# Kernel tuning notes

Hardware: AMD Instinct MI355X
Metric: run time of the kernel (lower is better)

## Reference

```python
import jax, jax.numpy as jnp
import numpy as np

N_NODES = 100000
DEG = 16
N_EDGES = N_NODES * DEG
D_IN = 128
D_OUT = 128


def setup_inputs() -> dict:
    key = jax.random.key(0)
    k1, k2, k3 = jax.random.split(key, 3)
    X = jax.random.normal(k1, (N_NODES, D_IN), dtype=jnp.float32)
    weights = jax.random.normal(k2, (D_IN, D_OUT), dtype=jnp.float32) * (1.0 / np.sqrt(D_OUT))
    # fixed-degree CSR: row i owns edges [i*DEG, (i+1)*DEG)
    row_pointers = (jnp.arange(N_NODES + 1, dtype=jnp.int32) * DEG)
    column_index = jax.random.randint(k3, (N_EDGES,), 0, N_NODES, dtype=jnp.int32)
    # TC-GNN kernel-scheduling metadata (no effect on math)
    blockPartition = jnp.zeros((N_NODES // DEG,), dtype=jnp.int32)
    edgeToColumn = jnp.zeros((N_EDGES,), dtype=jnp.int32)
    edgeToRow = jnp.zeros((N_EDGES,), dtype=jnp.int32)
    return {"X": X, "weights": weights, "row_pointers": row_pointers,
            "column_index": column_index, "blockPartition": blockPartition,
            "edgeToColumn": edgeToColumn, "edgeToRow": edgeToRow}


def _csr_spmm(feat, row_pointers, column_index):
    # out[i] = sum_{e in row i} feat[column_index[e]]  (unweighted SpMM)
    n = row_pointers.shape[0] - 1
    e = column_index.shape[0]
    # map each edge to its source row via searchsorted on the CSR pointer array
    row_ids = jnp.searchsorted(row_pointers, jnp.arange(e, dtype=row_pointers.dtype), side='right') - 1
    gathered = feat[column_index]  # [E, D]
    return jax.ops.segment_sum(gathered, row_ids, num_segments=n)


def reference(X, weights, row_pointers, column_index, blockPartition, edgeToColumn, edgeToRow):
    X_prime = jnp.matmul(X, weights)                      # [N, D_OUT] dense GEMM
    return _csr_spmm(X_prime, row_pointers, column_index)  # [N, D_OUT] neighbor sum
```

## Files before the change

### kernel.cpp

```cpp
#include <hip/hip_runtime.h>
#include <hip/hip_bf16.h>

#define N_NODES 100000
#define DEG 16
#define D 128

typedef __bf16 bf16x8 __attribute__((ext_vector_type(8)));
typedef float f32x4 __attribute__((ext_vector_type(4)));

__device__ __forceinline__ unsigned pk2(float a, float b) {
  union { __bf16 h[2]; unsigned u; } x;
  x.h[0] = (__bf16)a; x.h[1] = (__bf16)b;
  return x.u;
}

__device__ __forceinline__ int swz(int row, int k) {
  return (row << 7) + (k ^ ((row & 7) << 3));
}

__global__ void k_convW(const float* __restrict__ W, ushort* __restrict__ Wt) {
  int pos = (blockIdx.x << 8) + threadIdx.x;
  int k = pos >> 7, n = pos & 127;
  union { __bf16 h; ushort u; } c;
  c.h = (__bf16)W[pos];
  Wt[swz(n, k)] = c.u;
}

__global__ __launch_bounds__(256, 2) void k_gemm(const float* __restrict__ X,
                                                 const ushort* __restrict__ Wt,
                                                 ushort* __restrict__ Xp) {
  __shared__ __align__(16) ushort Ws[128 * 128];
  const int tid = threadIdx.x;
  const int row0 = blockIdx.x << 7;
  const int wave = tid >> 6;
  const int lane = tid & 63;
  const int lhi = lane >> 4;
  const int llo = lane & 15;

  {
    const uint4* src = (const uint4*)Wt;
    uint4* dst = (uint4*)Ws;
#pragma unroll
    for (int j = 0; j < 8; ++j) dst[(j << 8) + tid] = src[(j << 8) + tid];
  }

  float4 xa[2][4][2];
#pragma unroll
  for (int m = 0; m < 2; ++m) {
    int row = row0 + (wave << 5) + (m << 4) + llo;
    const float* rp = X + row * D + (lhi << 3);
    bool ok = row < N_NODES;
#pragma unroll
    for (int t = 0; t < 4; ++t) {
      xa[m][t][0] = ok ? *(const float4*)(rp + (t << 5)) : make_float4(0.f, 0.f, 0.f, 0.f);
      xa[m][t][1] = ok ? *(const float4*)(rp + (t << 5) + 4) : make_float4(0.f, 0.f, 0.f, 0.f);
    }
  }
  __syncthreads();

  f32x4 acc[2][8];
#pragma unroll
  for (int m = 0; m < 2; ++m)
#pragma unroll
    for (int n = 0; n < 8; ++n)
      acc[m][n] = (f32x4){0.f, 0.f, 0.f, 0.f};

#pragma unroll
  for (int t = 0; t < 4; ++t) {
    const int k0 = (t << 5) + (lhi << 3);
    bf16x8 a[2], b[8];
#pragma unroll
    for (int m = 0; m < 2; ++m) {
      float4 p = xa[m][t][0], q = xa[m][t][1];
      bf16x8 v;
      v[0] = (__bf16)p.x; v[1] = (__bf16)p.y; v[2] = (__bf16)p.z; v[3] = (__bf16)p.w;
      v[4] = (__bf16)q.x; v[5] = (__bf16)q.y; v[6] = (__bf16)q.z; v[7] = (__bf16)q.w;
      a[m] = v;
    }
#pragma unroll
    for (int n = 0; n < 8; ++n)
      b[n] = *(const bf16x8*)(Ws + swz((n << 4) + llo, k0));
#pragma unroll
    for (int m = 0; m < 2; ++m)
#pragma unroll
      for (int n = 0; n < 8; ++n)
        acc[m][n] = __builtin_amdgcn_mfma_f32_16x16x32_bf16(a[m], b[n], acc[m][n], 0, 0, 0);
  }

#pragma unroll
  for (int m = 0; m < 2; ++m) {
#pragma unroll
    for (int r = 0; r < 4; ++r) {
      int row = row0 + (wave << 5) + (m << 4) + (lhi << 2) + r;
      if (row < N_NODES) {
        uint4 v;
        v.x = pk2(acc[m][0][r], acc[m][1][r]);
        v.y = pk2(acc[m][2][r], acc[m][3][r]);
        v.z = pk2(acc[m][4][r], acc[m][5][r]);
        v.w = pk2(acc[m][6][r], acc[m][7][r]);
        *(uint4*)(Xp + row * D + (llo << 3)) = v;
      }
    }
  }
}

__global__ __launch_bounds__(256) void k_spmm(const ushort* __restrict__ Xp,
                                              const int* __restrict__ ci,
                                              float* __restrict__ out) {
  const int wave = threadIdx.x >> 6;
  const int lane = threadIdx.x & 63;
  const int row = (blockIdx.x << 2) + wave;
  if (row >= N_NODES) return;
  const int g = lane >> 4;
  const int j = lane & 15;

  int idx = 0;
  if (lane < DEG) idx = __builtin_nontemporal_load(ci + row * DEG + lane);

  uint4 v[4];
#pragma unroll
  for (int e = 0; e < 4; ++e) {
    int col = __shfl(idx, (g << 2) + e);
    v[e] = *(const uint4*)(Xp + col * D + (j << 3));
  }

  float acc[8];
#pragma unroll
  for (int n = 0; n < 8; ++n) acc[n] = 0.f;
#pragma unroll
  for (int e = 0; e < 4; ++e) {
    acc[0] += __uint_as_float(v[e].x << 16);
    acc[1] += __uint_as_float(v[e].x & 0xffff0000u);
    acc[2] += __uint_as_float(v[e].y << 16);
    acc[3] += __uint_as_float(v[e].y & 0xffff0000u);
    acc[4] += __uint_as_float(v[e].z << 16);
    acc[5] += __uint_as_float(v[e].z & 0xffff0000u);
    acc[6] += __uint_as_float(v[e].w << 16);
    acc[7] += __uint_as_float(v[e].w & 0xffff0000u);
  }

#pragma unroll
  for (int n = 0; n < 8; ++n) {
    acc[n] += __shfl_xor(acc[n], 16);
    acc[n] += __shfl_xor(acc[n], 32);
  }

  float* op = out + row * D + (g << 5) + j;
  __builtin_nontemporal_store(acc[(g << 1)], op);
  __builtin_nontemporal_store(acc[(g << 1) + 1], op + 16);
}

extern "C" void kernel_launch(void* const* d_in, const int* in_sizes, int n_in,
                              void* d_out, int out_size, void* d_ws, size_t ws_size,
                              hipStream_t stream) {
  const float* X = (const float*)d_in[0];
  const float* W = (const float*)d_in[1];
  const int* ci = (const int*)d_in[3];

  ushort* Wt = (ushort*)d_ws;
  ushort* Xp = (ushort*)d_ws + 128 * 128;
  float* out = (float*)d_out;

  k_convW<<<64, 256, 0, stream>>>(W, Wt);
  k_gemm<<<(N_NODES + 127) / 128, 256, 0, stream>>>(X, Wt, Xp);
  k_spmm<<<N_NODES / 4, 256, 0, stream>>>(Xp, ci, out);
}
```

Measured before the change: 83.45 us.

## Halve GEMM rows per block and make SpMM persistent with index prefetch

The GEMM now handles 64 rows per block instead of 128, with one M-tile per wave, higher launch-bounds occupancy and nontemporal X loads. Each block still loads the whole 32KB W tile into shared memory, so twice as many blocks repeat that copy. The SpMM becomes a grid-stride persistent kernel with 2048 blocks that prefetches the next row's column indices while gathering the current row. The aims are better latency hiding in the GEMM and less block launch overhead in the SpMM, at the cost of extra redundant W staging and fewer waves in flight for the gather.

```diff
diff --git a/kernel.cpp b/kernel.cpp
--- a/kernel.cpp
+++ b/kernel.cpp
@@ -4,9 +4,11 @@
 #define N_NODES 100000
 #define DEG 16
 #define D 128
+#define SPMM_BLOCKS 2048
 
 typedef __bf16 bf16x8 __attribute__((ext_vector_type(8)));
 typedef float f32x4 __attribute__((ext_vector_type(4)));
+typedef float f32x4v __attribute__((ext_vector_type(4)));
 
 __device__ __forceinline__ unsigned pk2(float a, float b) {
   union { __bf16 h[2]; unsigned u; } x;
@@ -26,12 +28,12 @@
   Wt[swz(n, k)] = c.u;
 }
 
-__global__ __launch_bounds__(256, 2) void k_gemm(const float* __restrict__ X,
+__global__ __launch_bounds__(256, 4) void k_gemm(const float* __restrict__ X,
                                                  const ushort* __restrict__ Wt,
                                                  ushort* __restrict__ Xp) {
   __shared__ __align__(16) ushort Ws[128 * 128];
   const int tid = threadIdx.x;
-  const int row0 = blockIdx.x << 7;
+  const int row0 = blockIdx.x << 6;
   const int wave = tid >> 6;
   const int lane = tid & 63;
   const int lhi = lane >> 4;
@@ -44,62 +46,51 @@
     for (int j = 0; j < 8; ++j) dst[(j << 8) + tid] = src[(j << 8) + tid];
   }
 
-  float4 xa[2][4][2];
-#pragma unroll
-  for (int m = 0; m < 2; ++m) {
-    int row = row0 + (wave << 5) + (m << 4) + llo;
+  bf16x8 af[4];
+  {
+    int row = row0 + (wave << 4) + llo;
     const float* rp = X + row * D + (lhi << 3);
     bool ok = row < N_NODES;
+    f32x4v t0[4], t1[4];
 #pragma unroll
     for (int t = 0; t < 4; ++t) {
-      xa[m][t][0] = ok ? *(const float4*)(rp + (t << 5)) : make_float4(0.f, 0.f, 0.f, 0.f);
-      xa[m][t][1] = ok ? *(const float4*)(rp + (t << 5) + 4) : make_float4(0.f, 0.f, 0.f, 0.f);
+      t0[t] = ok ? __builtin_nontemporal_load((const f32x4v*)(rp + (t << 5))) : (f32x4v){0.f, 0.f, 0.f, 0.f};
+      t1[t] = ok ? __builtin_nontemporal_load((const f32x4v*)(rp + (t << 5) + 4)) : (f32x4v){0.f, 0.f, 0.f, 0.f};
+    }
+#pragma unroll
+    for (int t = 0; t < 4; ++t) {
+      bf16x8 v;
+      v[0] = (__bf16)t0[t][0]; v[1] = (__bf16)t0[t][1]; v[2] = (__bf16)t0[t][2]; v[3] = (__bf16)t0[t][3];
+      v[4] = (__bf16)t1[t][0]; v[5] = (__bf16)t1[t][1]; v[6] = (__bf16)t1[t][2]; v[7] = (__bf16)t1[t][3];
+      af[t] = v;
     }
   }
   __syncthreads();
 
-  f32x4 acc[2][8];
+  f32x4 acc[8];
 #pragma unroll
-  for (int m = 0; m < 2; ++m)
-#pragma unroll
-    for (int n = 0; n < 8; ++n)
-      acc[m][n] = (f32x4){0.f, 0.f, 0.f, 0.f};
+  for (int n = 0; n < 8; ++n) acc[n] = (f32x4){0.f, 0.f, 0.f, 0.f};
 
 #pragma unroll
   for (int t = 0; t < 4; ++t) {
     const int k0 = (t << 5) + (lhi << 3);
-    bf16x8 a[2], b[8];
 #pragma unroll
-    for (int m = 0; m < 2; ++m) {
-      float4 p = xa[m][t][0], q = xa[m][t][1];
-      bf16x8 v;
-      v[0] = (__bf16)p.x; v[1] = (__bf16)p.y; v[2] = (__bf16)p.z; v[3] = (__bf16)p.w;
-      v[4] = (__bf16)q.x; v[5] = (__bf16)q.y; v[6] = (__bf16)q.z; v[7] = (__bf16)q.w;
-      a[m] = v;
+    for (int n = 0; n < 8; ++n) {
+      bf16x8 b = *(const bf16x8*)(Ws + swz((n << 4) + llo, k0));
+      acc[n] = __builtin_amdgcn_mfma_f32_16x16x32_bf16(af[t], b, acc[n], 0, 0, 0);
     }
-#pragma unroll
-    for (int n = 0; n < 8; ++n)
-      b[n] = *(const bf16x8*)(Ws + swz((n << 4) + llo, k0));
-#pragma unroll
-    for (int m = 0; m < 2; ++m)
-#pragma unroll
-      for (int n = 0; n < 8; ++n)
-        acc[m][n] = __builtin_amdgcn_mfma_f32_16x16x32_bf16(a[m], b[n], acc[m][n], 0, 0, 0);
   }
 
 #pragma unroll
-  for (int m = 0; m < 2; ++m) {
-#pragma unroll
-    for (int r = 0; r < 4; ++r) {
-      int row = row0 + (wave << 5) + (m << 4) + (lhi << 2) + r;
-      if (row < N_NODES) {
-        uint4 v;
-        v.x = pk2(acc[m][0][r], acc[m][1][r]);
-        v.y = pk2(acc[m][2][r], acc[m][3][r]);
-        v.z = pk2(acc[m][4][r], acc[m][5][r]);
-        v.w = pk2(acc[m][6][r], acc[m][7][r]);
-        *(uint4*)(Xp + row * D + (llo << 3)) = v;
-      }
+  for (int r = 0; r < 4; ++r) {
+    int row = row0 + (wave << 4) + (lhi << 2) + r;
+    if (row < N_NODES) {
+      uint4 v;
+      v.x = pk2(acc[0][r], acc[1][r]);
+      v.y = pk2(acc[2][r], acc[3][r]);
+      v.z = pk2(acc[4][r], acc[5][r]);
+      v.w = pk2(acc[6][r], acc[7][r]);
+      *(uint4*)(Xp + row * D + (llo << 3)) = v;
     }
   }
 }
@@ -109,45 +100,56 @@
                                               float* __restrict__ out) {
   const int wave = threadIdx.x >> 6;
   const int lane = threadIdx.x & 63;
-  const int row = (blockIdx.x << 2) + wave;
-  if (row >= N_NODES) return;
   const int g = lane >> 4;
   const int j = lane & 15;
+  const int nw = SPMM_BLOCKS << 2;
+  int row = (blockIdx.x << 2) + wave;
 
   int idx = 0;
   if (lane < DEG) idx = __builtin_nontemporal_load(ci + row * DEG + lane);
 
-  uint4 v[4];
+  while (true) {
+    int nrow = row + nw;
+    int nidx = 0;
+    if (nrow < N_NODES && lane < DEG)
+      nidx = __builtin_nontemporal_load(ci + nrow * DEG + lane);
+
+    uint4 v[4];
 #pragma unroll
-  for (int e = 0; e < 4; ++e) {
-    int col = __shfl(idx, (g << 2) + e);
-    v[e] = *(const uint4*)(Xp + col * D + (j << 3));
-  }
+    for (int e = 0; e < 4; ++e) {
+      int c = __shfl(idx, (g << 2) + e);
+      v[e] = *(const uint4*)(Xp + c * D + (j << 3));
+    }
 
-  float acc[8];
+    float acc[8];
 #pragma unroll
-  for (int n = 0; n < 8; ++n) acc[n] = 0.f;
+    for (int n = 0; n < 8; ++n) acc[n] = 0.f;
 #pragma unroll
-  for (int e = 0; e < 4; ++e) {
-    acc[0] += __uint_as_float(v[e].x << 16);
-    acc[1] += __uint_as_float(v[e].x & 0xffff0000u);
-    acc[2] += __uint_as_float(v[e].y << 16);
-    acc[3] += __uint_as_float(v[e].y & 0xffff0000u);
-    acc[4] += __uint_as_float(v[e].z << 16);
-    acc[5] += __uint_as_float(v[e].z & 0xffff0000u);
-    acc[6] += __uint_as_float(v[e].w << 16);
-    acc[7] += __uint_as_float(v[e].w & 0xffff0000u);
-  }
+    for (int e = 0; e < 4; ++e) {
+      acc[0] += __uint_as_float(v[e].x << 16);
+      acc[1] += __uint_as_float(v[e].x & 0xffff0000u);
+      acc[2] += __uint_as_float(v[e].y << 16);
+      acc[3] += __uint_as_float(v[e].y & 0xffff0000u);
+      acc[4] += __uint_as_float(v[e].z << 16);
+      acc[5] += __uint_as_float(v[e].z & 0xffff0000u);
+      acc[6] += __uint_as_float(v[e].w << 16);
+      acc[7] += __uint_as_float(v[e].w & 0xffff0000u);
+    }
 
 #pragma unroll
-  for (int n = 0; n < 8; ++n) {
-    acc[n] += __shfl_xor(acc[n], 16);
-    acc[n] += __shfl_xor(acc[n], 32);
+    for (int n = 0; n < 8; ++n) {
+      acc[n] += __shfl_xor(acc[n], 16);
+      acc[n] += __shfl_xor(acc[n], 32);
+    }
+
+    float* op = out + row * D + (g << 5) + j;
+    __builtin_nontemporal_store(acc[(g << 1)], op);
+    __builtin_nontemporal_store(acc[(g << 1) + 1], op + 16);
+
+    if (nrow >= N_NODES) break;
+    row = nrow;
+    idx = nidx;
   }
-
-  float* op = out + row * D + (g << 5) + j;
-  __builtin_nontemporal_store(acc[(g << 1)], op);
-  __builtin_nontemporal_store(acc[(g << 1) + 1], op + 16);
 }
 
 extern "C" void kernel_launch(void* const* d_in, const int* in_sizes, int n_in,
@@ -162,6 +164,6 @@
   float* out = (float*)d_out;
 
   k_convW<<<64, 256, 0, stream>>>(W, Wt);
-  k_gemm<<<(N_NODES + 127) / 128, 256, 0, stream>>>(X, Wt, Xp);
-  k_spmm<<<N_NODES / 4, 256, 0, stream>>>(Xp, ci, out);
+  k_gemm<<<(N_NODES + 63) / 64, 256, 0, stream>>>(X, Wt, Xp);
+  k_spmm<<<SPMM_BLOCKS, 256, 0, stream>>>(Xp, ci, out);
 }
```

Result: slower. 89.55 us (+7.3%).
